# Optimization experiments

Measured on AMD Instinct MI355X. Metric: run time of the kernel, lower is better.

## Reference

```python
import jax, jax.numpy as jnp
import numpy as np
import math

N_HEADS = 8
SLOPE = 0.01      # LeakyReLU negative slope (torch default)
EPS_K = 1e-6      # numerical stabilizer in softmax kernel transformation
EPS_N = 1e-5      # GraphNorm eps
TAU = 1.0
N_NODES = 50000
DIM = 64          # in = hidden = out channels (head dim)
M_FEAT = 30       # nb_random_features
N_EDGES = 800000


def softmax_kernel(data, proj, is_query):
    # data: [N, H, D], proj: [M, D] -> [N, H, M] positive random features
    dn = 1.0 / math.sqrt(math.sqrt(data.shape[-1]))
    ratio = 1.0 / math.sqrt(proj.shape[0])
    dd = jnp.einsum('nhd,md->nhm', dn * data, proj)
    diag = jnp.sum(jnp.square(data), axis=-1, keepdims=True) * (dn * dn * 0.5)
    if is_query:
        stab = jnp.max(dd, axis=-1, keepdims=True)            # per (n,h)
    else:
        stab = jnp.max(dd, axis=(0, 2), keepdims=True)        # per h, over n and m
    return ratio * (jnp.exp(dd - diag - stab) + EPS_K)


def nodeformer_conv(x, Wq, bq, Wk, bk, Wv, bv, Wo, bo, proj):
    # x: [N, C]; Wq/Wk/Wv: [C, H*D]; Wo: [H*D, D_out]; proj: [M, D]
    N = x.shape[0]
    H = N_HEADS
    D = Wq.shape[1] // H
    inv = 1.0 / math.sqrt(TAU)
    q = ((x @ Wq + bq).reshape(N, H, D)) * inv
    k = ((x @ Wk + bk).reshape(N, H, D)) * inv
    v = (x @ Wv + bv).reshape(N, H, D)
    qp = softmax_kernel(q, proj, True)    # [N,H,M]
    kp = softmax_kernel(k, proj, False)   # [N,H,M]
    kvs = jnp.einsum('nhm,nhd->hmd', kp, v)          # O(N) linear attention
    num = jnp.einsum('nhm,hmd->nhd', qp, kvs)
    den = jnp.einsum('nhm,hm->nh', qp, jnp.sum(kp, axis=0))
    z = num / den[..., None]                          # [N,H,D]
    return z.reshape(N, H * D) @ Wo + bo


def graph_norm(x, gamma, beta, alpha):
    # single graph: normalize over all nodes; alpha = learnable mean scale
    mu = jnp.mean(x, axis=0, keepdims=True)
    xc = x - alpha * mu
    var = jnp.mean(jnp.square(xc), axis=0, keepdims=True)
    return gamma * xc * jax.lax.rsqrt(var + EPS_N) + beta


def leaky_relu(x):
    return jnp.where(x >= 0, x, SLOPE * x)


def setup_inputs() -> dict:
    key = jax.random.key(0)
    ks = jax.random.split(key, 12)
    HD = N_HEADS * DIM
    s = 0.02
    inp = {
        'patch_embs': jax.random.normal(ks[0], (N_NODES, DIM), jnp.float32),
        'edge_index': jax.random.randint(ks[1], (2, N_EDGES), 0, N_NODES),
        'edge_attr': jax.random.normal(ks[2], (N_EDGES, 8), jnp.float32),
        'Wq': jax.random.normal(ks[3], (3, DIM, HD), jnp.float32) * s,
        'Wk': jax.random.normal(ks[4], (3, DIM, HD), jnp.float32) * s,
        'Wv': jax.random.normal(ks[5], (3, DIM, HD), jnp.float32) * s,
        'Wo': jax.random.normal(ks[6], (3, HD, DIM), jnp.float32) * s,
        'bq': jnp.zeros((3, HD), jnp.float32),
        'bk': jnp.zeros((3, HD), jnp.float32),
        'bv': jnp.zeros((3, HD), jnp.float32),
        'bo': jnp.zeros((3, DIM), jnp.float32),
        'P': jax.random.normal(ks[7], (3, M_FEAT, DIM), jnp.float32),
        'gamma': jnp.ones((3, DIM), jnp.float32),
        'beta': jnp.zeros((3, DIM), jnp.float32),
        'alpha': jnp.ones((3, DIM), jnp.float32),
    }
    return inp


def reference(patch_embs, edge_index, edge_attr, Wq, Wk, Wv, Wo, bq, bk, bv, bo, P, gamma, beta, alpha):
    x = nodeformer_conv(patch_embs, Wq[0], bq[0], Wk[0], bk[0], Wv[0], bv[0], Wo[0], bo[0], P[0])
    x = graph_norm(leaky_relu(x), gamma[0], beta[0], alpha[0])
    x = nodeformer_conv(x, Wq[1], bq[1], Wk[1], bk[1], Wv[1], bv[1], Wo[1], bo[1], P[1])
    x = graph_norm(leaky_relu(x), gamma[1], beta[1], alpha[1])
    x = nodeformer_conv(x, Wq[2], bq[2], Wk[2], bk[2], Wv[2], bv[2], Wo[2], bo[2], P[2])
    x = graph_norm(x, gamma[2], beta[2], alpha[2])
    return x
```

## Files before the change

### kernel.cpp

```cpp
#include <hip/hip_runtime.h>
#include <math.h>


namespace {

constexpr int N    = 50000;
constexpr int C    = 64;
constexpr int H    = 8;
constexpr int HD   = 512;
constexpr int M    = 30;

constexpr int NBK  = 128;
constexpr int NGK  = N / 16;
constexpr int NBQ  = 1024;
constexpr int NGQ8 = N / 8;
constexpr int PSTR = 2016;

__device__ constexpr double DN    = 0.35355339059327373;
__device__ constexpr double RATIO = 0.18257418583505536;
__device__ constexpr double EPSK  = 1e-6;
__device__ constexpr double EPSN  = 1e-5;

__device__ __forceinline__ void kah(double& s, double& c, double v) {
  double y = v - c; double t = s + y; c = (t - s) - y; s = t;
}

__global__ __launch_bounds__(256)
void k_wp(const float* __restrict__ Wk, const float* __restrict__ bk,
          const float* __restrict__ Wq, const float* __restrict__ bq,
          const float* __restrict__ P, float* __restrict__ wp,
          float* __restrict__ bp) {
  const int blk = blockIdx.x, side = blk >> 3, h = blk & 7, t = threadIdx.x;
  const float* W  = side ? Wq : Wk;
  const float* bb = side ? bq : bk;
  for (int s = t; s < 1920; s += 256) {
    const int m = s >> 6, c = s & 63;
    double a = 0.0;
    for (int d = 0; d < 64; ++d)
      a = fma((double)W[c * HD + h * 64 + d], (double)P[m * 64 + d], a);
    wp[((size_t)(side * 8 + h) * 30 + m) * 64 + c] = (float)(a * DN);
  }
  if (t < 30) {
    double a = 0.0;
    for (int d = 0; d < 64; ++d)
      a = fma((double)bb[h * 64 + d], (double)P[t * 64 + d], a);
    bp[(side * 8 + h) * 30 + t] = (float)(a * DN);
  }
}

__global__ __launch_bounds__(256, 4)
void k_kv(const float* __restrict__ x32,
          const float* __restrict__ Wk, const float* __restrict__ bk,
          const float* __restrict__ Wv, const float* __restrict__ bv,
          const float* __restrict__ wp, const float* __restrict__ bp,
          float* __restrict__ partial) {
  __shared__ __align__(16) float wvs[4096];
  __shared__ __align__(16) float wpk[30 * 68];
  __shared__ __align__(16) float xs[16 * 68];
  __shared__ __align__(16) float vsd[16 * 68];
  __shared__ float kplV[30 * 16];
  __shared__ float diag[16];
  __shared__ float bpk[30];
  const int t = threadIdx.x, i0 = t >> 6, c0 = t & 63;
  const int h = blockIdx.x >> 7, b = blockIdx.x & (NBK - 1), hb = h * 64;

  for (int s = t; s < 4096; s += 256)
    wvs[s] = Wv[(s >> 6) * HD + hb + (s & 63)];
  for (int s = t; s < 1920; s += 256)
    wpk[(s >> 6) * 68 + (s & 63)] = wp[(size_t)h * 1920 + s];
  if (t < 30) bpk[t] = bp[h * 30 + t];
  const float bk0 = bk[hb + c0], bv0 = bv[hb + c0];
  float acc8[8];
#pragma unroll
  for (int k = 0; k < 8; ++k) acc8[k] = 0.0f;
  float ssv = 0.0f, ses = 0.0f, runmax = -3.0e38f;
  __syncthreads();

  for (int g = b; g < NGK; g += NBK) {
    const int n0 = g * 16;
    __syncthreads();
#pragma unroll
    for (int u = 0; u < 4; ++u)
      xs[(i0 + 4 * u) * 68 + c0] = x32[(size_t)(n0 + i0 + 4 * u) * C + c0];
    __syncthreads();
    float ka[4], va[4];
#pragma unroll
    for (int u = 0; u < 4; ++u) { ka[u] = bk0; va[u] = bv0; }
#pragma unroll 4
    for (int c4 = 0; c4 < 16; ++c4) {
      float4 xv[4];
#pragma unroll
      for (int u = 0; u < 4; ++u)
        xv[u] = reinterpret_cast<const float4*>(xs + (i0 + 4 * u) * 68)[c4];
#pragma unroll
      for (int j = 0; j < 4; ++j) {
        const int c = c4 * 4 + j;
        const float wk_ = Wk[c * HD + hb + c0];
        const float wv_ = wvs[c * 64 + c0];
        const float xj0 = (j == 0) ? xv[0].x : (j == 1) ? xv[0].y : (j == 2) ? xv[0].z : xv[0].w;
        const float xj1 = (j == 0) ? xv[1].x : (j == 1) ? xv[1].y : (j == 2) ? xv[1].z : xv[1].w;
        const float xj2 = (j == 0) ? xv[2].x : (j == 1) ? xv[2].y : (j == 2) ? xv[2].z : xv[2].w;
        const float xj3 = (j == 0) ? xv[3].x : (j == 1) ? xv[3].y : (j == 2) ? xv[3].z : xv[3].w;
        ka[0] = fmaf(xj0, wk_, ka[0]); va[0] = fmaf(xj0, wv_, va[0]);
        ka[1] = fmaf(xj1, wk_, ka[1]); va[1] = fmaf(xj1, wv_, va[1]);
        ka[2] = fmaf(xj2, wk_, ka[2]); va[2] = fmaf(xj2, wv_, va[2]);
        ka[3] = fmaf(xj3, wk_, ka[3]); va[3] = fmaf(xj3, wv_, va[3]);
      }
    }
#pragma unroll
    for (int u = 0; u < 4; ++u) {
      vsd[(i0 + 4 * u) * 68 + c0] = va[u];
      float s = ka[u] * ka[u];
#pragma unroll
      for (int off = 32; off; off >>= 1) s += __shfl_xor(s, off, 64);
      if (c0 == 0) diag[i0 + 4 * u] = s * 0.0625f;
      ssv += va[u];
    }
    __syncthreads();
#pragma unroll
    for (int rep = 0; rep < 2; ++rep) {
      const int item = t + rep * 256;
      if (item < 480) {
        const int dm = item >> 4, di = item & 15;
        float a = bpk[dm];
#pragma unroll 4
        for (int c4 = 0; c4 < 16; ++c4) {
          const float4 xv = reinterpret_cast<const float4*>(xs + di * 68)[c4];
          const float4 wv = reinterpret_cast<const float4*>(wpk + dm * 68)[c4];
          a = fmaf(xv.x, wv.x, a); a = fmaf(xv.y, wv.y, a);
          a = fmaf(xv.z, wv.z, a); a = fmaf(xv.w, wv.w, a);
        }
        runmax = fmaxf(runmax, a);
        kplV[dm * 16 + di] = __expf(a - diag[di]);
      }
    }
    __syncthreads();
    if (t < 30) {
      float gsum = 0.0f;
#pragma unroll
      for (int i = 0; i < 16; ++i) gsum += kplV[t * 16 + i];
      ses += gsum;
    }
    float vr[16];
#pragma unroll
    for (int i = 0; i < 16; ++i) vr[i] = vsd[i * 68 + c0];
#pragma unroll
    for (int k = 0; k < 8; ++k) {
      const int s = t + (k << 8);
      if (s < 1920) {
        const int m = s >> 6;
        float gsum = acc8[k];
#pragma unroll
        for (int i = 0; i < 16; ++i)
          gsum = fmaf(kplV[m * 16 + i], vr[i], gsum);
        acc8[k] = gsum;
      }
    }
  }
  const size_t base = (size_t)blockIdx.x * PSTR;
  __syncthreads();
  xs[t] = ssv;
  vsd[t] = runmax;
  __syncthreads();
  if (t < 64) partial[base + 1950 + t] = xs[t] + xs[t + 64] + xs[t + 128] + xs[t + 192];
  for (int off = 128; off; off >>= 1) {
    if (t < off) vsd[t] = fmaxf(vsd[t], vsd[t + off]);
    __syncthreads();
  }
  if (t == 0) partial[base + 2014] = vsd[0];
  if (t < 30) partial[base + 1920 + t] = ses;
#pragma unroll
  for (int k = 0; k < 8; ++k) {
    const int s = t + (k << 8);
    if (s < 1920) partial[base + s] = acc8[k];
  }
}

__global__ __launch_bounds__(256)
void k_redkv(const float* __restrict__ partial, const float* __restrict__ Wo,
             double* __restrict__ ksumg, float* __restrict__ Gg32) {
  const int h = blockIdx.x, t = threadIdx.x;
  __shared__ float red[256];
  __shared__ double svt[64];
  __shared__ double kvls[M * 64];
  __shared__ double escs;
  const size_t hb = (size_t)h * NBK;
  red[t] = (t < NBK) ? partial[(hb + t) * PSTR + 2014] : -3.0e38f;
  __syncthreads();
  for (int off = 128; off; off >>= 1) {
    if (t < off) red[t] = fmaxf(red[t], red[t + off]);
    __syncthreads();
  }
  if (t == 0) escs = exp(-(double)red[0]);
  __syncthreads();
  const double esc = escs;
  if (t < 64) {
    double s = 0.0;
    for (int b = 0; b < NBK; ++b) s += (double)partial[(hb + b) * PSTR + 1950 + t];
    svt[t] = s;
  } else if (t < 64 + M) {
    const int m = t - 64;
    double s = 0.0;
    for (int b = 0; b < NBK; ++b) s += (double)partial[(hb + b) * PSTR + 1920 + m];
    ksumg[h * M + m] = RATIO * (esc * s + EPSK * (double)N);
  }
  __syncthreads();
#pragma unroll
  for (int k = 0; k < 8; ++k) {
    const int sidx = t + (k << 8);
    if (sidx < M * 64) {
      double s = 0.0;
      for (int b = 0; b < NBK; ++b) s += (double)partial[(hb + b) * PSTR + sidx];
      kvls[sidx] = RATIO * (esc * s + EPSK * svt[sidx & 63]);
    }
  }
  __syncthreads();
#pragma unroll
  for (int k = 0; k < 8; ++k) {
    const int sidx = t + (k << 8);
    if (sidx < M * 64) {
      const int m = sidx >> 6, c = sidx & 63;
      double a = 0.0;
      for (int d = 0; d < 64; ++d)
        a = fma(kvls[m * 64 + d], (double)Wo[(h * 64 + d) * 64 + c], a);
      Gg32[(size_t)h * 1920 + sidx] = (float)a;
    }
  }
}

template <int MODE>
__global__ __launch_bounds__(256, 4)
void k_q(const float* __restrict__ x32,
         const float* __restrict__ Wq, const float* __restrict__ bq,
         const float* __restrict__ wp, const float* __restrict__ bp,
         const double* __restrict__ ksumg, const float* __restrict__ Gg32,
         const float* __restrict__ bo, int do_leaky, int H0,
         double* __restrict__ y, double* __restrict__ psum) {
  __shared__ __align__(16) float wpq[60 * 68];
  __shared__ float Gl[2][1920];
  __shared__ __align__(16) float xs[8 * 68];
  __shared__ float  qpl[60 * 8];
  __shared__ float  stabd[16];
  __shared__ float  diagd[16];
  __shared__ double rdend[16];
  __shared__ double ksl[60];
  __shared__ float  bpq[60];
  __shared__ double red[256];
  const int t = threadIdx.x, i0 = t >> 6, c0 = t & 63;

  for (int s = t; s < 3840; s += 256) {
    const int hh = s / 1920, r = s - hh * 1920;
    wpq[(hh * 30 + (r >> 6)) * 68 + (r & 63)] = wp[(size_t)(8 + H0 + hh) * 1920 + r];
    Gl[hh][r] = Gg32[(size_t)(H0 + hh) * 1920 + r];
  }
  if (t < 60) {
    ksl[t] = ksumg[H0 * 30 + t];
    bpq[t] = bp[(8 + H0) * 30 + t];
  }
  const float bqA = bq[H0 * 64 + c0];
  const float bqB = bq[H0 * 64 + 64 + c0];
  const double bo0 = (double)bo[c0];
  double sy = 0.0, sy2 = 0.0;
  __syncthreads();

  for (int g = blockIdx.x; g < NGQ8; g += NBQ) {
    const int n0 = g * 8;
    xs[i0 * 68 + c0]       = x32[(size_t)(n0 + i0) * C + c0];
    xs[(i0 + 4) * 68 + c0] = x32[(size_t)(n0 + i0 + 4) * C + c0];
    __syncthreads();
    float aq0 = bqA, aq1 = bqB, aq2 = bqA, aq3 = bqB;
#pragma unroll 4
    for (int c4 = 0; c4 < 16; ++c4) {
      const float4 xa = reinterpret_cast<const float4*>(xs + i0 * 68)[c4];
      const float4 xb = reinterpret_cast<const float4*>(xs + (i0 + 4) * 68)[c4];
#pragma unroll
      for (int j = 0; j < 4; ++j) {
        const int c = c4 * 4 + j;
        const float wA = Wq[c * HD + H0 * 64 + c0];
        const float wB = Wq[c * HD + H0 * 64 + 64 + c0];
        const float xaj = (j == 0) ? xa.x : (j == 1) ? xa.y : (j == 2) ? xa.z : xa.w;
        const float xbj = (j == 0) ? xb.x : (j == 1) ? xb.y : (j == 2) ? xb.z : xb.w;
        aq0 = fmaf(xaj, wA, aq0); aq1 = fmaf(xaj, wB, aq1);
        aq2 = fmaf(xbj, wA, aq2); aq3 = fmaf(xbj, wB, aq3);
      }
    }
    {
      float s0 = aq0 * aq0, s1 = aq1 * aq1, s2 = aq2 * aq2, s3 = aq3 * aq3;
#pragma unroll
      for (int off = 32; off; off >>= 1) {
        s0 += __shfl_xor(s0, off, 64); s1 += __shfl_xor(s1, off, 64);
        s2 += __shfl_xor(s2, off, 64); s3 += __shfl_xor(s3, off, 64);
      }
      if (c0 == 0) {
        diagd[i0 * 2]           = s0 * 0.0625f;
        diagd[i0 * 2 + 1]       = s1 * 0.0625f;
        diagd[(i0 + 4) * 2]     = s2 * 0.0625f;
        diagd[(i0 + 4) * 2 + 1] = s3 * 0.0625f;
      }
    }
#pragma unroll
    for (int rep = 0; rep < 2; ++rep) {
      const int item = t + rep * 256;
      if (item < 480) {
        const int j = item >> 3, i = item & 7;
        float a = bpq[j];
#pragma unroll 4
        for (int c4 = 0; c4 < 16; ++c4) {
          const float4 xv = reinterpret_cast<const float4*>(xs + i * 68)[c4];
          const float4 wv = reinterpret_cast<const float4*>(wpq + j * 68)[c4];
          a = fmaf(xv.x, wv.x, a); a = fmaf(xv.y, wv.y, a);
          a = fmaf(xv.z, wv.z, a); a = fmaf(xv.w, wv.w, a);
        }
        qpl[item] = a;
      }
    }
    __syncthreads();
    if (t < 16) {
      const int hh = t >> 3, i = t & 7;
      float mx = qpl[(hh * 30) * 8 + i];
      for (int m = 1; m < 30; ++m) mx = fmaxf(mx, qpl[(hh * 30 + m) * 8 + i]);
      stabd[t] = mx;
    }
    __syncthreads();
#pragma unroll
    for (int rep = 0; rep < 2; ++rep) {
      const int item = t + rep * 256;
      if (item < 480) {
        const int j = item >> 3, i = item & 7;
        const int hh = (j >= 30) ? 1 : 0;
        qpl[item] = 0.18257418583505536f *
                    (__expf((qpl[item] - diagd[i * 2 + hh]) - stabd[hh * 8 + i]) + 1e-6f);
      }
    }
    __syncthreads();
    if (t < 16) {
      const int hh = t >> 3, i = t & 7;
      double den = 0.0;
      for (int m = 0; m < 30; ++m)
        den = fma((double)qpl[(hh * 30 + m) * 8 + i], ksl[hh * 30 + m], den);
      rdend[i * 2 + hh] = 1.0 / den;
    }
    __syncthreads();
    double acc_a = 0.0, acc_b = 0.0;
#pragma unroll
    for (int hh = 0; hh < 2; ++hh) {
      const float* g = Gl[hh] + c0;
      const int jb = hh * 30;
      double sa = 0.0, sb = 0.0;
      for (int m = 0; m < 30; ++m) {
        const double gv = (double)g[m * 64];
        sa = fma((double)qpl[(jb + m) * 8 + i0], gv, sa);
        sb = fma((double)qpl[(jb + m) * 8 + i0 + 4], gv, sb);
      }
      acc_a = fma(sa, rdend[i0 * 2 + hh], acc_a);
      acc_b = fma(sb, rdend[(i0 + 4) * 2 + hh], acc_b);
    }
    const size_t ia = (size_t)(n0 + i0) * C + c0;
    const size_t ib = (size_t)(n0 + i0 + 4) * C + c0;
    if (MODE == 0) {
      y[ia] = bo0 + acc_a;
      y[ib] = bo0 + acc_b;
    } else if (MODE == 1) {
      y[ia] += acc_a;
      y[ib] += acc_b;
    } else {
      double va = y[ia] + acc_a, vb = y[ib] + acc_b;
      if (do_leaky) {
        va = (va >= 0.0) ? va : 0.01 * va;
        vb = (vb >= 0.0) ? vb : 0.01 * vb;
      }
      y[ia] = va; y[ib] = vb;
      sy += va + vb;
      sy2 = fma(va, va, sy2);
      sy2 = fma(vb, vb, sy2);
    }
  }
  if (MODE == 2) {
    __syncthreads();
    red[t] = sy;
    __syncthreads();
    if (t < 64) psum[(size_t)blockIdx.x * 128 + t] =
        red[t] + red[t + 64] + red[t + 128] + red[t + 192];
    __syncthreads();
    red[t] = sy2;
    __syncthreads();
    if (t < 64) psum[(size_t)blockIdx.x * 128 + 64 + t] =
        red[t] + red[t + 64] + red[t + 128] + red[t + 192];
  }
}

__global__ void k_norm_params(const double* __restrict__ psum,
                              const float* __restrict__ gamma, const float* __restrict__ beta,
                              const float* __restrict__ alpha, double* __restrict__ nparam) {
  const int t = threadIdx.x;
  __shared__ double m1l[64], m2l[64];
  if (t < 64) {
    double s = 0, c = 0;
    for (int b = 0; b < NBQ; ++b) kah(s, c, psum[(size_t)b * 128 + t]);
    m1l[t] = s - c;
  } else if (t < 128) {
    const int ci = t - 64;
    double s = 0, c = 0;
    for (int b = 0; b < NBQ; ++b) kah(s, c, psum[(size_t)b * 128 + 64 + ci]);
    m2l[ci] = s - c;
  }
  __syncthreads();
  if (t < 64) {
    const double mu = m1l[t] / (double)N;
    const double m2 = m2l[t] / (double)N;
    const double al = (double)alpha[t];
    double var = m2 - (2.0 * al - al * al) * mu * mu;
    if (var < 0.0) var = 0.0;
    nparam[t]       = al * mu;
    nparam[64 + t]  = (double)gamma[t] / sqrt(var + EPSN);
    nparam[128 + t] = (double)beta[t];
  }
}

__global__ void k_cast(const double* __restrict__ yv, const double* __restrict__ nparam,
                       float* __restrict__ dst) {
  const int total = N * C;
  for (int i = blockIdx.x * blockDim.x + threadIdx.x; i < total; i += gridDim.x * blockDim.x) {
    const int c = i & 63;
    dst[i] = (float)((yv[i] - nparam[c]) * nparam[64 + c] + nparam[128 + c]);
  }
}

}

extern "C" void kernel_launch(void* const* d_in, const int* in_sizes, int n_in,
                              void* d_out, int out_size, void* d_ws, size_t ws_size,
                              hipStream_t stream) {
  const float* patch = (const float*)d_in[0];
  const float* Wq = (const float*)d_in[3];
  const float* Wk = (const float*)d_in[4];
  const float* Wv = (const float*)d_in[5];
  const float* Wo = (const float*)d_in[6];
  const float* bq = (const float*)d_in[7];
  const float* bk = (const float*)d_in[8];
  const float* bv = (const float*)d_in[9];
  const float* bo = (const float*)d_in[10];
  const float* P  = (const float*)d_in[11];
  const float* ga = (const float*)d_in[12];
  const float* be = (const float*)d_in[13];
  const float* al = (const float*)d_in[14];
  float* out = (float*)d_out;

  char* wsb = (char*)d_ws;
  double* y      = (double*)wsb;   wsb += (size_t)N * C * 8;
  double* psum   = (double*)wsb;   wsb += (size_t)NBQ * 128 * 8;
  double* nparam = (double*)wsb;   wsb += 192 * 8;
  double* ksumg  = (double*)wsb;   wsb += (size_t)H * M * 8;
  float*  x32    = (float*)wsb;    wsb += (size_t)N * C * 4;
  float*  partial= (float*)wsb;    wsb += (size_t)(H * NBK) * PSTR * 4;
  float*  G32    = (float*)wsb;    wsb += (size_t)H * M * 64 * 4;
  float*  wpf    = (float*)wsb;    wsb += (size_t)2 * H * M * 64 * 4;
  float*  bpf    = (float*)wsb;    wsb += (size_t)2 * H * M * 4;

  for (int L = 0; L < 3; ++L) {
    const float* wq  = Wq + (size_t)L * C * HD;
    const float* wk  = Wk + (size_t)L * C * HD;
    const float* wv  = Wv + (size_t)L * C * HD;
    const float* wo  = Wo + (size_t)L * HD * C;
    const float* bq_ = bq + (size_t)L * HD;
    const float* bk_ = bk + (size_t)L * HD;
    const float* bv_ = bv + (size_t)L * HD;
    const float* bo_ = bo + (size_t)L * C;
    const float* p   = P  + (size_t)L * M * C;
    const int leaky = (L < 2) ? 1 : 0;
    const float* xcur = (L == 0) ? patch : x32;

    k_wp<<<16, 256, 0, stream>>>(wk, bk_, wq, bq_, p, wpf, bpf);
    k_kv<<<H * NBK, 256, 0, stream>>>(xcur, wk, bk_, wv, bv_, wpf, bpf, partial);
    k_redkv<<<H, 256, 0, stream>>>(partial, wo, ksumg, G32);

    k_q<0><<<NBQ, 256, 0, stream>>>(xcur, wq, bq_, wpf, bpf, ksumg, G32, bo_,
                                    leaky, 0, y, psum);
    k_q<1><<<NBQ, 256, 0, stream>>>(xcur, wq, bq_, wpf, bpf, ksumg, G32, bo_,
                                    leaky, 2, y, psum);
    k_q<1><<<NBQ, 256, 0, stream>>>(xcur, wq, bq_, wpf, bpf, ksumg, G32, bo_,
                                    leaky, 4, y, psum);
    k_q<2><<<NBQ, 256, 0, stream>>>(xcur, wq, bq_, wpf, bpf, ksumg, G32, bo_,
                                    leaky, 6, y, psum);

    k_norm_params<<<1, 128, 0, stream>>>(psum, ga + (size_t)L * C, be + (size_t)L * C,
                                         al + (size_t)L * C, nparam);
    k_cast<<<512, 256, 0, stream>>>(y, nparam, (L < 2) ? x32 : out);
  }
}
```

Measured before the change: 2.363 ms.

## Compute query squared-norm diagonal in k_kv and read it in k_q

```diff
diff --git a/kernel.cpp b/kernel.cpp
--- a/kernel.cpp
+++ b/kernel.cpp
@@ -52,8 +52,9 @@
 void k_kv(const float* __restrict__ x32,
           const float* __restrict__ Wk, const float* __restrict__ bk,
           const float* __restrict__ Wv, const float* __restrict__ bv,
+          const float* __restrict__ Wq, const float* __restrict__ bq,
           const float* __restrict__ wp, const float* __restrict__ bp,
-          float* __restrict__ partial) {
+          float* __restrict__ partial, float* __restrict__ diagq) {
   __shared__ __align__(16) float wvs[4096];
   __shared__ __align__(16) float wpk[30 * 68];
   __shared__ __align__(16) float xs[16 * 68];
@@ -69,7 +70,7 @@
   for (int s = t; s < 1920; s += 256)
     wpk[(s >> 6) * 68 + (s & 63)] = wp[(size_t)h * 1920 + s];
   if (t < 30) bpk[t] = bp[h * 30 + t];
-  const float bk0 = bk[hb + c0], bv0 = bv[hb + c0];
+  const float bk0 = bk[hb + c0], bv0 = bv[hb + c0], bq0 = bq[hb + c0];
   float acc8[8];
 #pragma unroll
   for (int k = 0; k < 8; ++k) acc8[k] = 0.0f;
@@ -83,9 +84,9 @@
     for (int u = 0; u < 4; ++u)
       xs[(i0 + 4 * u) * 68 + c0] = x32[(size_t)(n0 + i0 + 4 * u) * C + c0];
     __syncthreads();
-    float ka[4], va[4];
-#pragma unroll
-    for (int u = 0; u < 4; ++u) { ka[u] = bk0; va[u] = bv0; }
+    float ka[4], va[4], qa[4];
+#pragma unroll
+    for (int u = 0; u < 4; ++u) { ka[u] = bk0; va[u] = bv0; qa[u] = bq0; }
 #pragma unroll 4
     for (int c4 = 0; c4 < 16; ++c4) {
       float4 xv[4];
@@ -96,24 +97,32 @@
       for (int j = 0; j < 4; ++j) {
         const int c = c4 * 4 + j;
         const float wk_ = Wk[c * HD + hb + c0];
+        const float wq_ = Wq[c * HD + hb + c0];
         const float wv_ = wvs[c * 64 + c0];
         const float xj0 = (j == 0) ? xv[0].x : (j == 1) ? xv[0].y : (j == 2) ? xv[0].z : xv[0].w;
         const float xj1 = (j == 0) ? xv[1].x : (j == 1) ? xv[1].y : (j == 2) ? xv[1].z : xv[1].w;
         const float xj2 = (j == 0) ? xv[2].x : (j == 1) ? xv[2].y : (j == 2) ? xv[2].z : xv[2].w;
         const float xj3 = (j == 0) ? xv[3].x : (j == 1) ? xv[3].y : (j == 2) ? xv[3].z : xv[3].w;
-        ka[0] = fmaf(xj0, wk_, ka[0]); va[0] = fmaf(xj0, wv_, va[0]);
-        ka[1] = fmaf(xj1, wk_, ka[1]); va[1] = fmaf(xj1, wv_, va[1]);
-        ka[2] = fmaf(xj2, wk_, ka[2]); va[2] = fmaf(xj2, wv_, va[2]);
-        ka[3] = fmaf(xj3, wk_, ka[3]); va[3] = fmaf(xj3, wv_, va[3]);
+        ka[0] = fmaf(xj0, wk_, ka[0]); va[0] = fmaf(xj0, wv_, va[0]); qa[0] = fmaf(xj0, wq_, qa[0]);
+        ka[1] = fmaf(xj1, wk_, ka[1]); va[1] = fmaf(xj1, wv_, va[1]); qa[1] = fmaf(xj1, wq_, qa[1]);
+        ka[2] = fmaf(xj2, wk_, ka[2]); va[2] = fmaf(xj2, wv_, va[2]); qa[2] = fmaf(xj2, wq_, qa[2]);
+        ka[3] = fmaf(xj3, wk_, ka[3]); va[3] = fmaf(xj3, wv_, va[3]); qa[3] = fmaf(xj3, wq_, qa[3]);
       }
     }
 #pragma unroll
     for (int u = 0; u < 4; ++u) {
       vsd[(i0 + 4 * u) * 68 + c0] = va[u];
       float s = ka[u] * ka[u];
-#pragma unroll
-      for (int off = 32; off; off >>= 1) s += __shfl_xor(s, off, 64);
-      if (c0 == 0) diag[i0 + 4 * u] = s * 0.0625f;
+      float sq = qa[u] * qa[u];
+#pragma unroll
+      for (int off = 32; off; off >>= 1) {
+        s  += __shfl_xor(s,  off, 64);
+        sq += __shfl_xor(sq, off, 64);
+      }
+      if (c0 == 0) {
+        diag[i0 + 4 * u] = s * 0.0625f;
+        diagq[(size_t)h * N + n0 + i0 + 4 * u] = sq * 0.0625f;
+      }
       ssv += va[u];
     }
     __syncthreads();
@@ -231,8 +240,8 @@
 template <int MODE>
 __global__ __launch_bounds__(256, 4)
 void k_q(const float* __restrict__ x32,
-         const float* __restrict__ Wq, const float* __restrict__ bq,
          const float* __restrict__ wp, const float* __restrict__ bp,
+         const float* __restrict__ diagq,
          const double* __restrict__ ksumg, const float* __restrict__ Gg32,
          const float* __restrict__ bo, int do_leaky, int H0,
          double* __restrict__ y, double* __restrict__ psum) {
@@ -245,7 +254,6 @@
   __shared__ double rdend[16];
   __shared__ double ksl[60];
   __shared__ float  bpq[60];
-  __shared__ double red[256];
   const int t = threadIdx.x, i0 = t >> 6, c0 = t & 63;
 
   for (int s = t; s < 3840; s += 256) {
@@ -257,8 +265,6 @@
     ksl[t] = ksumg[H0 * 30 + t];
     bpq[t] = bp[(8 + H0) * 30 + t];
   }
-  const float bqA = bq[H0 * 64 + c0];
-  const float bqB = bq[H0 * 64 + 64 + c0];
   const double bo0 = (double)bo[c0];
   double sy = 0.0, sy2 = 0.0;
   __syncthreads();
@@ -267,37 +273,11 @@
     const int n0 = g * 8;
     xs[i0 * 68 + c0]       = x32[(size_t)(n0 + i0) * C + c0];
     xs[(i0 + 4) * 68 + c0] = x32[(size_t)(n0 + i0 + 4) * C + c0];
-    __syncthreads();
-    float aq0 = bqA, aq1 = bqB, aq2 = bqA, aq3 = bqB;
-#pragma unroll 4
-    for (int c4 = 0; c4 < 16; ++c4) {
-      const float4 xa = reinterpret_cast<const float4*>(xs + i0 * 68)[c4];
-      const float4 xb = reinterpret_cast<const float4*>(xs + (i0 + 4) * 68)[c4];
-#pragma unroll
-      for (int j = 0; j < 4; ++j) {
-        const int c = c4 * 4 + j;
-        const float wA = Wq[c * HD + H0 * 64 + c0];
-        const float wB = Wq[c * HD + H0 * 64 + 64 + c0];
-        const float xaj = (j == 0) ? xa.x : (j == 1) ? xa.y : (j == 2) ? xa.z : xa.w;
-        const float xbj = (j == 0) ? xb.x : (j == 1) ? xb.y : (j == 2) ? xb.z : xb.w;
-        aq0 = fmaf(xaj, wA, aq0); aq1 = fmaf(xaj, wB, aq1);
-        aq2 = fmaf(xbj, wA, aq2); aq3 = fmaf(xbj, wB, aq3);
-      }
-    }
-    {
-      float s0 = aq0 * aq0, s1 = aq1 * aq1, s2 = aq2 * aq2, s3 = aq3 * aq3;
-#pragma unroll
-      for (int off = 32; off; off >>= 1) {
-        s0 += __shfl_xor(s0, off, 64); s1 += __shfl_xor(s1, off, 64);
-        s2 += __shfl_xor(s2, off, 64); s3 += __shfl_xor(s3, off, 64);
-      }
-      if (c0 == 0) {
-        diagd[i0 * 2]           = s0 * 0.0625f;
-        diagd[i0 * 2 + 1]       = s1 * 0.0625f;
-        diagd[(i0 + 4) * 2]     = s2 * 0.0625f;
-        diagd[(i0 + 4) * 2 + 1] = s3 * 0.0625f;
-      }
-    }
+    if (t < 16) {
+      const int hh = t >> 3, i = t & 7;
+      diagd[i * 2 + hh] = diagq[(size_t)(H0 + hh) * N + n0 + i];
+    }
+    __syncthreads();
 #pragma unroll
     for (int rep = 0; rep < 2; ++rep) {
       const int item = t + rep * 256;
@@ -376,6 +356,7 @@
     }
   }
   if (MODE == 2) {
+    double* red = reinterpret_cast<double*>(wpq);
     __syncthreads();
     red[t] = sy;
     __syncthreads();
@@ -456,6 +437,7 @@
   float*  G32    = (float*)wsb;    wsb += (size_t)H * M * 64 * 4;
   float*  wpf    = (float*)wsb;    wsb += (size_t)2 * H * M * 64 * 4;
   float*  bpf    = (float*)wsb;    wsb += (size_t)2 * H * M * 4;
+  float*  diagq  = (float*)wsb;    wsb += (size_t)H * N * 4;
 
   for (int L = 0; L < 3; ++L) {
     const float* wq  = Wq + (size_t)L * C * HD;
@@ -471,16 +453,17 @@
     const float* xcur = (L == 0) ? patch : x32;
 
     k_wp<<<16, 256, 0, stream>>>(wk, bk_, wq, bq_, p, wpf, bpf);
-    k_kv<<<H * NBK, 256, 0, stream>>>(xcur, wk, bk_, wv, bv_, wpf, bpf, partial);
+    k_kv<<<H * NBK, 256, 0, stream>>>(xcur, wk, bk_, wv, bv_, wq, bq_,
+                                      wpf, bpf, partial, diagq);
     k_redkv<<<H, 256, 0, stream>>>(partial, wo, ksumg, G32);
 
-    k_q<0><<<NBQ, 256, 0, stream>>>(xcur, wq, bq_, wpf, bpf, ksumg, G32, bo_,
+    k_q<0><<<NBQ, 256, 0, stream>>>(xcur, wpf, bpf, diagq, ksumg, G32, bo_,
                                     leaky, 0, y, psum);
-    k_q<1><<<NBQ, 256, 0, stream>>>(xcur, wq, bq_, wpf, bpf, ksumg, G32, bo_,
+    k_q<1><<<NBQ, 256, 0, stream>>>(xcur, wpf, bpf, diagq, ksumg, G32, bo_,
                                     leaky, 2, y, psum);
-    k_q<1><<<NBQ, 256, 0, stream>>>(xcur, wq, bq_, wpf, bpf, ksumg, G32, bo_,
+    k_q<1><<<NBQ, 256, 0, stream>>>(xcur, wpf, bpf, diagq, ksumg, G32, bo_,
                                     leaky, 4, y, psum);
-    k_q<2><<<NBQ, 256, 0, stream>>>(xcur, wq, bq_, wpf, bpf, ksumg, G32, bo_,
+    k_q<2><<<NBQ, 256, 0, stream>>>(xcur, wpf, bpf, diagq, ksumg, G32, bo_,
                                     leaky, 6, y, psum);
 
     k_norm_params<<<1, 128, 0, stream>>>(psum, ga + (size_t)L * C, be + (size_t)L * C,
```

After: 3.753 ms. 58.8% more time.
